# Kernel optimization log

Hardware: AMD Instinct MI355X
Metric: run time of the kernel (lower is better)

Reference implementation:

```python
import jax, jax.numpy as jnp
import numpy as np

B, T, D, F, E = 4, 8192, 1024, 4096, 8


def setup_inputs() -> dict:
    key = jax.random.key(0)
    ks = jax.random.split(key, 5)
    s = 0.02
    return {
        "X": jax.random.normal(ks[0], (B, T, D), dtype=jnp.float32),
        "slots_w": jax.random.normal(ks[1], (E, D), dtype=jnp.float32) * s,
        "w1": jax.random.normal(ks[2], (E, F, D), dtype=jnp.float32) * s,
        "w3": jax.random.normal(ks[3], (E, F, D), dtype=jnp.float32) * s,
        "w2": jax.random.normal(ks[4], (E, D, F), dtype=jnp.float32) * s,
    }


def reference(X, slots_w, w1, w3, w2):
    # logits: [B,T,E]
    logits = jnp.einsum("btd,ed->bte", X, slots_w)
    dispatch_w = jax.nn.softmax(logits, axis=1)  # softmax over tokens
    combine_w = jax.nn.softmax(logits, axis=2)   # softmax over experts
    # slots: one D-vector per expert per batch -> [B,E,D]
    slots = jnp.einsum("bte,btd->bed", dispatch_w, X)
    # SwiGLU FFN batched over experts
    h = jax.nn.silu(jnp.einsum("bed,efd->bef", slots, w1)) * jnp.einsum("bed,efd->bef", slots, w3)
    y = jnp.einsum("bef,edf->bed", h, w2)  # [B,E,D]
    # combine back to tokens: [B,T,D]
    return jnp.einsum("bte,bed->btd", combine_w, y)
```

## Files before the change

kernel.cpp:

```cpp
#include <hip/hip_runtime.h>
#include <math.h>

#define NB 4
#define NT 8192
#define ND 1024
#define NF 4096
#define NE 8

#define DCH 128
#define DTOK 64
#define K7_CHB 256
#define K7_TOK (NT / K7_CHB)

typedef float v4f __attribute__((ext_vector_type(4)));

__device__ __forceinline__ float4 ntload4(const float* p) {
  v4f v = __builtin_nontemporal_load((const v4f*)p);
  return make_float4(v.x, v.y, v.z, v.w);
}
__device__ __forceinline__ void ntstore4(float* p, float4 a) {
  v4f v = {a.x, a.y, a.z, a.w};
  __builtin_nontemporal_store(v, (v4f*)p);
}

__device__ __forceinline__ float dot4(float4 a, float4 b) {
  return a.x * b.x + a.y * b.y + a.z * b.z + a.w * b.w;
}

__device__ __forceinline__ float reduce8(float v0, float v1, float v2, float v3,
                                         float v4, float v5, float v6, float v7,
                                         int lane) {
  const bool b0 = lane & 1;
  float s, u0, u1, u2, u3;
  s = b0 ? v0 : v1; u0 = (b0 ? v1 : v0) + __shfl_xor(s, 1);
  s = b0 ? v2 : v3; u1 = (b0 ? v3 : v2) + __shfl_xor(s, 1);
  s = b0 ? v4 : v5; u2 = (b0 ? v5 : v4) + __shfl_xor(s, 1);
  s = b0 ? v6 : v7; u3 = (b0 ? v7 : v6) + __shfl_xor(s, 1);
  const bool b1 = lane & 2;
  float w0, w1;
  s = b1 ? u0 : u1; w0 = (b1 ? u1 : u0) + __shfl_xor(s, 2);
  s = b1 ? u2 : u3; w1 = (b1 ? u3 : u2) + __shfl_xor(s, 2);
  const bool b2 = lane & 4;
  s = b2 ? w0 : w1; float x = (b2 ? w1 : w0) + __shfl_xor(s, 4);
  x += __shfl_xor(x, 8);
  x += __shfl_xor(x, 16);
  x += __shfl_xor(x, 32);
  return x;
}

__global__ __launch_bounds__(256, 2) void k_dispatch(const float* __restrict__ X,
                                                     const float* __restrict__ sw,
                                                     float* __restrict__ logits,
                                                     float* __restrict__ partial,
                                                     float* __restrict__ Lpart) {
  const int tid = threadIdx.x;
  const int lane = tid & 63, wave = tid >> 6;
  const int b = blockIdx.x >> 7;
  const int chunk = blockIdx.x & 127;
  const int t0 = chunk * DTOK;

  float4 swr[NE];
#pragma unroll
  for (int e = 0; e < NE; ++e)
    swr[e] = *(const float4*)(sw + (size_t)e * ND + tid * 4);

  __shared__ float wred[4][8][8];
  __shared__ float pwt[8][8];
  __shared__ float lsum[8][8];

  const float* xb = X + ((size_t)b * NT + t0) * ND + tid * 4;
  float4 Xc[8], Xn[8];
#pragma unroll
  for (int k = 0; k < 8; ++k) Xc[k] = ntload4(xb + (size_t)k * ND);

  float4 acc[NE];
#pragma unroll
  for (int e = 0; e < NE; ++e) acc[e] = make_float4(0.f, 0.f, 0.f, 0.f);
  float Lacc = 0.f;

  for (int g = 0; g < 8; ++g) {
    if (g < 7) {
#pragma unroll
      for (int k = 0; k < 8; ++k)
        Xn[k] = ntload4(xb + (size_t)((g + 1) * 8 + k) * ND);
    }
#pragma unroll
    for (int k = 0; k < 8; ++k) {
      float p0 = dot4(Xc[k], swr[0]), p1 = dot4(Xc[k], swr[1]);
      float p2 = dot4(Xc[k], swr[2]), p3 = dot4(Xc[k], swr[3]);
      float p4 = dot4(Xc[k], swr[4]), p5 = dot4(Xc[k], swr[5]);
      float p6 = dot4(Xc[k], swr[6]), p7 = dot4(Xc[k], swr[7]);
      float r = reduce8(p0, p1, p2, p3, p4, p5, p6, p7, lane);
      if (lane < 8) wred[wave][k][lane] = r;
    }
    asm volatile("s_waitcnt lgkmcnt(0)" ::: "memory");
    __builtin_amdgcn_s_barrier();
    if (wave == 0) {
      const int t = lane >> 3, e = lane & 7;
      if (lane < 64) {
        float lg = wred[0][t][e] + wred[1][t][e] + wred[2][t][e] + wred[3][t][e];
        logits[((size_t)b * NT + t0 + g * 8 + t) * NE + e] = lg;
        float ex = expf(lg);
        pwt[t][e] = ex;
        Lacc += ex;
      }
    }
    asm volatile("s_waitcnt lgkmcnt(0)" ::: "memory");
    __builtin_amdgcn_s_barrier();
#pragma unroll
    for (int k = 0; k < 8; ++k) {
      float4 pa = *(const float4*)&pwt[k][0];
      float4 pb = *(const float4*)&pwt[k][4];
      float4 x = Xc[k];
      acc[0].x += pa.x * x.x; acc[0].y += pa.x * x.y; acc[0].z += pa.x * x.z; acc[0].w += pa.x * x.w;
      acc[1].x += pa.y * x.x; acc[1].y += pa.y * x.y; acc[1].z += pa.y * x.z; acc[1].w += pa.y * x.w;
      acc[2].x += pa.z * x.x; acc[2].y += pa.z * x.y; acc[2].z += pa.z * x.z; acc[2].w += pa.z * x.w;
      acc[3].x += pa.w * x.x; acc[3].y += pa.w * x.y; acc[3].z += pa.w * x.z; acc[3].w += pa.w * x.w;
      acc[4].x += pb.x * x.x; acc[4].y += pb.x * x.y; acc[4].z += pb.x * x.z; acc[4].w += pb.x * x.w;
      acc[5].x += pb.y * x.x; acc[5].y += pb.y * x.y; acc[5].z += pb.y * x.z; acc[5].w += pb.y * x.w;
      acc[6].x += pb.z * x.x; acc[6].y += pb.z * x.y; acc[6].z += pb.z * x.z; acc[6].w += pb.z * x.w;
      acc[7].x += pb.w * x.x; acc[7].y += pb.w * x.y; acc[7].z += pb.w * x.z; acc[7].w += pb.w * x.w;
    }
    asm volatile("s_waitcnt lgkmcnt(0)" ::: "memory");
    __builtin_amdgcn_s_barrier();
#pragma unroll
    for (int k = 0; k < 8; ++k) Xc[k] = Xn[k];
  }

  float* pout = partial + (size_t)blockIdx.x * (NE * ND) + tid * 4;
#pragma unroll
  for (int e = 0; e < NE; ++e) *(float4*)(pout + e * ND) = acc[e];

  if (wave == 0 && lane < 64) lsum[lane >> 3][lane & 7] = Lacc;
  __syncthreads();
  if (tid < 8) {
    float s = 0.f;
#pragma unroll
    for (int t = 0; t < 8; ++t) s += lsum[t][tid];
    Lpart[(size_t)blockIdx.x * NE + tid] = s;
  }
}

__global__ __launch_bounds__(256, 4) void k_slots_reduce(const float* __restrict__ partial,
                                                         const float* __restrict__ Lpart,
                                                         float* __restrict__ slots) {
  const int col = blockIdx.x * 256 + threadIdx.x;
  const int b = col >> 13;
  const int ed = col & 8191;
  const int e = ed >> 10;
  const float* p = partial + (size_t)b * DCH * (NE * ND) + ed;
  float s = 0.f;
#pragma unroll 8
  for (int c = 0; c < DCH; ++c) s += p[(size_t)c * NE * ND];
  const float* lp = Lpart + (size_t)b * DCH * NE + e;
  float Ls = 0.f;
#pragma unroll 8
  for (int c = 0; c < DCH; ++c) Ls += lp[c * NE];
  slots[col] = s / Ls;
}

__global__ __launch_bounds__(256, 8) void k_ffn1(const float* __restrict__ slots,
                                                 const float* __restrict__ w1,
                                                 const float* __restrict__ w3,
                                                 float* __restrict__ h) {
  __shared__ float4 s_sl[NB][ND / 4];
  const int tid = threadIdx.x;
  const int lane = tid & 63, wave = tid >> 6;
  const int e = blockIdx.x >> 8;
  const int f0 = (blockIdx.x & 255) * 16;
  for (int i = tid; i < NB * ND / 4; i += 256) {
    const int b = i >> 8, j = i & 255;
    s_sl[b][j] = ((const float4*)(slots + ((size_t)b * NE + e) * ND))[j];
  }
  __syncthreads();

  const float* w1e = w1 + (size_t)e * NF * ND;
  const float* w3e = w3 + (size_t)e * NF * ND;
  float4 W1c[4], W3c[4], W1n[4], W3n[4];
  {
    const int f = f0 + wave;
    const float* r1 = w1e + (size_t)f * ND;
    const float* r3 = w3e + (size_t)f * ND;
#pragma unroll
    for (int it = 0; it < 4; ++it) {
      W1c[it] = ntload4(r1 + (it * 64 + lane) * 4);
      W3c[it] = ntload4(r3 + (it * 64 + lane) * 4);
    }
  }
#pragma unroll
  for (int rg = 0; rg < 4; ++rg) {
    const int f = f0 + wave + rg * 4;
    if (rg < 3) {
      const float* r1 = w1e + (size_t)(f + 4) * ND;
      const float* r3 = w3e + (size_t)(f + 4) * ND;
#pragma unroll
      for (int it = 0; it < 4; ++it) {
        W1n[it] = ntload4(r1 + (it * 64 + lane) * 4);
        W3n[it] = ntload4(r3 + (it * 64 + lane) * 4);
      }
    }
    float a1[NB] = {0.f, 0.f, 0.f, 0.f}, a3[NB] = {0.f, 0.f, 0.f, 0.f};
#pragma unroll
    for (int it = 0; it < 4; ++it) {
      float4 x1 = W1c[it], x3 = W3c[it];
#pragma unroll
      for (int b = 0; b < NB; ++b) {
        float4 s = s_sl[b][it * 64 + lane];
        a1[b] += dot4(x1, s);
        a3[b] += dot4(x3, s);
      }
    }
    float x = reduce8(a1[0], a1[1], a1[2], a1[3],
                      a3[0], a3[1], a3[2], a3[3], lane);
    float other = __shfl_xor(x, 4);
    if (lane < 4) {
      const float sil = x / (1.f + expf(-x));
      h[((size_t)e * NB + lane) * NF + f] = sil * other;
    }
#pragma unroll
    for (int it = 0; it < 4; ++it) { W1c[it] = W1n[it]; W3c[it] = W3n[it]; }
  }
}

__global__ __launch_bounds__(256, 4) void k_ffn2(const float* __restrict__ h,
                                                 const float* __restrict__ w2,
                                                 float* __restrict__ y_part) {
  const int tid = threadIdx.x;
  const int lane = tid & 63, wave = tid >> 6;
  const int e = blockIdx.x >> 8;
  const int rem = blockIdx.x & 255;
  const int d0 = (rem >> 2) * 16;
  const int c = rem & 3;
  const int fb = c * 1024;

  const float* he = h + (size_t)e * NB * NF;
  const float* w2e = w2 + (size_t)e * ND * NF;
  const int r0 = d0 + wave * 4;

  float4 Wc[4], Wn[4], Hc[4], Hn[4];
  {
    const int pos = fb + lane * 4;
#pragma unroll
    for (int r = 0; r < 4; ++r) Wc[r] = ntload4(w2e + (size_t)(r0 + r) * NF + pos);
#pragma unroll
    for (int b = 0; b < NB; ++b) Hc[b] = *(const float4*)(he + (size_t)b * NF + pos);
  }
  float acc[4][NB];
#pragma unroll
  for (int r = 0; r < 4; ++r)
#pragma unroll
    for (int b = 0; b < NB; ++b) acc[r][b] = 0.f;

#pragma unroll
  for (int si = 0; si < 4; ++si) {
    if (si < 3) {
      const int pos = fb + (si + 1) * 256 + lane * 4;
#pragma unroll
      for (int r = 0; r < 4; ++r) Wn[r] = ntload4(w2e + (size_t)(r0 + r) * NF + pos);
#pragma unroll
      for (int b = 0; b < NB; ++b) Hn[b] = *(const float4*)(he + (size_t)b * NF + pos);
    }
#pragma unroll
    for (int r = 0; r < 4; ++r)
#pragma unroll
      for (int b = 0; b < NB; ++b) acc[r][b] += dot4(Wc[r], Hc[b]);
#pragma unroll
    for (int r = 0; r < 4; ++r) Wc[r] = Wn[r];
#pragma unroll
    for (int b = 0; b < NB; ++b) Hc[b] = Hn[b];
  }

  float x01 = reduce8(acc[0][0], acc[0][1], acc[0][2], acc[0][3],
                      acc[1][0], acc[1][1], acc[1][2], acc[1][3], lane);
  float x23 = reduce8(acc[2][0], acc[2][1], acc[2][2], acc[2][3],
                      acc[3][0], acc[3][1], acc[3][2], acc[3][3], lane);
  if (lane < 8) {
    const int b = lane & 3, r = lane >> 2;
    y_part[(((size_t)c * NB + b) * NE + e) * ND + r0 + r] = x01;
    y_part[(((size_t)c * NB + b) * NE + e) * ND + r0 + 2 + r] = x23;
  }
}

__global__ __launch_bounds__(256, 4) void k_combine(const float* __restrict__ logits,
                                                    const float* __restrict__ y_part,
                                                    float* __restrict__ out) {
  const int b = blockIdx.x >> 8;
  const int t0 = (blockIdx.x & 255) * K7_TOK;
  __shared__ float4 s_y[NE * ND / 4];
  const float4* yp = (const float4*)y_part;
  for (int i = threadIdx.x; i < NE * ND / 4; i += 256) {
    float4 a = yp[(size_t)(0 * NB + b) * 2048 + i];
    float4 c1 = yp[(size_t)(1 * NB + b) * 2048 + i];
    float4 c2 = yp[(size_t)(2 * NB + b) * 2048 + i];
    float4 c3 = yp[(size_t)(3 * NB + b) * 2048 + i];
    a.x += c1.x + c2.x + c3.x; a.y += c1.y + c2.y + c3.y;
    a.z += c1.z + c2.z + c3.z; a.w += c1.w + c2.w + c3.w;
    s_y[i] = a;
  }
  __shared__ float s_cw[K7_TOK][NE];
  if (threadIdx.x < K7_TOK) {
    const int t = t0 + threadIdx.x;
    const float* lg = logits + ((size_t)b * NT + t) * NE;
    float l[NE];
    float mx = -1e30f;
#pragma unroll
    for (int e = 0; e < NE; ++e) { l[e] = lg[e]; mx = fmaxf(mx, l[e]); }
    float s = 0.f;
#pragma unroll
    for (int e = 0; e < NE; ++e) { l[e] = expf(l[e] - mx); s += l[e]; }
    const float inv = 1.f / s;
#pragma unroll
    for (int e = 0; e < NE; ++e) s_cw[threadIdx.x][e] = l[e] * inv;
  }
  __syncthreads();
  for (int t = 0; t < K7_TOK; ++t) {
    float4 o = make_float4(0.f, 0.f, 0.f, 0.f);
#pragma unroll
    for (int e = 0; e < NE; ++e) {
      const float cw = s_cw[t][e];
      float4 yv = s_y[e * 256 + threadIdx.x];
      o.x += cw * yv.x; o.y += cw * yv.y; o.z += cw * yv.z; o.w += cw * yv.w;
    }
    ntstore4(out + ((size_t)b * NT + t0 + t) * ND + threadIdx.x * 4, o);
  }
}

extern "C" void kernel_launch(void* const* d_in, const int* in_sizes, int n_in,
                              void* d_out, int out_size, void* d_ws, size_t ws_size,
                              hipStream_t stream) {
  const float* X  = (const float*)d_in[0];
  const float* sw = (const float*)d_in[1];
  const float* w1 = (const float*)d_in[2];
  const float* w3 = (const float*)d_in[3];
  const float* w2 = (const float*)d_in[4];
  float* out = (float*)d_out;

  float* ws = (float*)d_ws;
  float* logits  = ws;
  float* partial = logits + (size_t)NB * NT * NE;
  float* Lpart   = partial + (size_t)NB * DCH * NE * ND;
  float* slots   = Lpart + (size_t)NB * DCH * NE;
  float* h       = slots + NB * NE * ND;
  float* y_part  = h + (size_t)NE * NB * NF;

  hipLaunchKernelGGL(k_dispatch, dim3(NB * DCH), dim3(256), 0, stream,
                     X, sw, logits, partial, Lpart);
  hipLaunchKernelGGL(k_slots_reduce, dim3(NB * NE * ND / 256), dim3(256), 0, stream,
                     partial, Lpart, slots);
  hipLaunchKernelGGL(k_ffn1, dim3(NE * (NF / 16)), dim3(256), 0, stream,
                     slots, w1, w3, h);
  hipLaunchKernelGGL(k_ffn2, dim3(NE * (ND / 16) * 4), dim3(256), 0, stream, h, w2, y_part);
  hipLaunchKernelGGL(k_combine, dim3(NB * K7_CHB), dim3(256), 0, stream, logits, y_part, out);
}
```

Baseline: 167.7 us.

## Double-buffer dispatch weights, keep combine y in registers, relax ffn1 launch bounds

In the dispatch kernel, the per-group exp weights go into a two-slot shared buffer, which lets the trailing barrier of each group iteration be removed. The combine kernel now holds the reduced expert outputs in registers per thread instead of staging them in shared memory, and reads the combine weights as vector loads. The occupancy hint on the first FFN kernel drops from 8 to 4 blocks per CU, giving it more registers. These are independent changes across three kernels. Removing the barrier relies on the double buffer preventing a write-after-read race on wred and pwt, and the lower occupancy may reduce latency hiding in ffn1.

```diff
diff --git a/kernel.cpp b/kernel.cpp
--- a/kernel.cpp
+++ b/kernel.cpp
@@ -65,7 +65,7 @@
     swr[e] = *(const float4*)(sw + (size_t)e * ND + tid * 4);
 
   __shared__ float wred[4][8][8];
-  __shared__ float pwt[8][8];
+  __shared__ float pwt[2][8][8];
   __shared__ float lsum[8][8];
 
   const float* xb = X + ((size_t)b * NT + t0) * ND + tid * 4;
@@ -79,6 +79,7 @@
   float Lacc = 0.f;
 
   for (int g = 0; g < 8; ++g) {
+    const int pb = g & 1;
     if (g < 7) {
 #pragma unroll
       for (int k = 0; k < 8; ++k)
@@ -97,32 +98,28 @@
     __builtin_amdgcn_s_barrier();
     if (wave == 0) {
       const int t = lane >> 3, e = lane & 7;
-      if (lane < 64) {
-        float lg = wred[0][t][e] + wred[1][t][e] + wred[2][t][e] + wred[3][t][e];
-        logits[((size_t)b * NT + t0 + g * 8 + t) * NE + e] = lg;
-        float ex = expf(lg);
-        pwt[t][e] = ex;
-        Lacc += ex;
-      }
+      float lg = wred[0][t][e] + wred[1][t][e] + wred[2][t][e] + wred[3][t][e];
+      logits[((size_t)b * NT + t0 + g * 8 + t) * NE + e] = lg;
+      float ex = expf(lg);
+      pwt[pb][t][e] = ex;
+      Lacc += ex;
     }
     asm volatile("s_waitcnt lgkmcnt(0)" ::: "memory");
     __builtin_amdgcn_s_barrier();
 #pragma unroll
     for (int k = 0; k < 8; ++k) {
-      float4 pa = *(const float4*)&pwt[k][0];
-      float4 pb = *(const float4*)&pwt[k][4];
+      float4 pa = *(const float4*)&pwt[pb][k][0];
+      float4 pbv = *(const float4*)&pwt[pb][k][4];
       float4 x = Xc[k];
       acc[0].x += pa.x * x.x; acc[0].y += pa.x * x.y; acc[0].z += pa.x * x.z; acc[0].w += pa.x * x.w;
       acc[1].x += pa.y * x.x; acc[1].y += pa.y * x.y; acc[1].z += pa.y * x.z; acc[1].w += pa.y * x.w;
       acc[2].x += pa.z * x.x; acc[2].y += pa.z * x.y; acc[2].z += pa.z * x.z; acc[2].w += pa.z * x.w;
       acc[3].x += pa.w * x.x; acc[3].y += pa.w * x.y; acc[3].z += pa.w * x.z; acc[3].w += pa.w * x.w;
-      acc[4].x += pb.x * x.x; acc[4].y += pb.x * x.y; acc[4].z += pb.x * x.z; acc[4].w += pb.x * x.w;
-      acc[5].x += pb.y * x.x; acc[5].y += pb.y * x.y; acc[5].z += pb.y * x.z; acc[5].w += pb.y * x.w;
-      acc[6].x += pb.z * x.x; acc[6].y += pb.z * x.y; acc[6].z += pb.z * x.z; acc[6].w += pb.z * x.w;
-      acc[7].x += pb.w * x.x; acc[7].y += pb.w * x.y; acc[7].z += pb.w * x.z; acc[7].w += pb.w * x.w;
-    }
-    asm volatile("s_waitcnt lgkmcnt(0)" ::: "memory");
-    __builtin_amdgcn_s_barrier();
+      acc[4].x += pbv.x * x.x; acc[4].y += pbv.x * x.y; acc[4].z += pbv.x * x.z; acc[4].w += pbv.x * x.w;
+      acc[5].x += pbv.y * x.x; acc[5].y += pbv.y * x.y; acc[5].z += pbv.y * x.z; acc[5].w += pbv.y * x.w;
+      acc[6].x += pbv.z * x.x; acc[6].y += pbv.z * x.y; acc[6].z += pbv.z * x.z; acc[6].w += pbv.z * x.w;
+      acc[7].x += pbv.w * x.x; acc[7].y += pbv.w * x.y; acc[7].z += pbv.w * x.z; acc[7].w += pbv.w * x.w;
+    }
 #pragma unroll
     for (int k = 0; k < 8; ++k) Xc[k] = Xn[k];
   }
@@ -131,7 +128,7 @@
 #pragma unroll
   for (int e = 0; e < NE; ++e) *(float4*)(pout + e * ND) = acc[e];
 
-  if (wave == 0 && lane < 64) lsum[lane >> 3][lane & 7] = Lacc;
+  if (wave == 0) lsum[lane >> 3][lane & 7] = Lacc;
   __syncthreads();
   if (tid < 8) {
     float s = 0.f;
@@ -159,7 +156,7 @@
   slots[col] = s / Ls;
 }
 
-__global__ __launch_bounds__(256, 8) void k_ffn1(const float* __restrict__ slots,
+__global__ __launch_bounds__(256, 4) void k_ffn1(const float* __restrict__ slots,
                                                  const float* __restrict__ w1,
                                                  const float* __restrict__ w3,
                                                  float* __restrict__ h) {
@@ -286,20 +283,24 @@
                                                     float* __restrict__ out) {
   const int b = blockIdx.x >> 8;
   const int t0 = (blockIdx.x & 255) * K7_TOK;
-  __shared__ float4 s_y[NE * ND / 4];
+  const int tid = threadIdx.x;
+
+  float4 yreg[NE];
   const float4* yp = (const float4*)y_part;
-  for (int i = threadIdx.x; i < NE * ND / 4; i += 256) {
-    float4 a = yp[(size_t)(0 * NB + b) * 2048 + i];
-    float4 c1 = yp[(size_t)(1 * NB + b) * 2048 + i];
-    float4 c2 = yp[(size_t)(2 * NB + b) * 2048 + i];
-    float4 c3 = yp[(size_t)(3 * NB + b) * 2048 + i];
+#pragma unroll
+  for (int e = 0; e < NE; ++e) {
+    float4 a = yp[(size_t)((0 * NB + b) * NE + e) * 256 + tid];
+    float4 c1 = yp[(size_t)((1 * NB + b) * NE + e) * 256 + tid];
+    float4 c2 = yp[(size_t)((2 * NB + b) * NE + e) * 256 + tid];
+    float4 c3 = yp[(size_t)((3 * NB + b) * NE + e) * 256 + tid];
     a.x += c1.x + c2.x + c3.x; a.y += c1.y + c2.y + c3.y;
     a.z += c1.z + c2.z + c3.z; a.w += c1.w + c2.w + c3.w;
-    s_y[i] = a;
-  }
+    yreg[e] = a;
+  }
+
   __shared__ float s_cw[K7_TOK][NE];
-  if (threadIdx.x < K7_TOK) {
-    const int t = t0 + threadIdx.x;
+  if (tid < K7_TOK) {
+    const int t = t0 + tid;
     const float* lg = logits + ((size_t)b * NT + t) * NE;
     float l[NE];
     float mx = -1e30f;
@@ -310,18 +311,23 @@
     for (int e = 0; e < NE; ++e) { l[e] = expf(l[e] - mx); s += l[e]; }
     const float inv = 1.f / s;
 #pragma unroll
-    for (int e = 0; e < NE; ++e) s_cw[threadIdx.x][e] = l[e] * inv;
+    for (int e = 0; e < NE; ++e) s_cw[tid][e] = l[e] * inv;
   }
   __syncthreads();
+
   for (int t = 0; t < K7_TOK; ++t) {
+    float4 ca = *(const float4*)&s_cw[t][0];
+    float4 cb = *(const float4*)&s_cw[t][4];
     float4 o = make_float4(0.f, 0.f, 0.f, 0.f);
-#pragma unroll
-    for (int e = 0; e < NE; ++e) {
-      const float cw = s_cw[t][e];
-      float4 yv = s_y[e * 256 + threadIdx.x];
-      o.x += cw * yv.x; o.y += cw * yv.y; o.z += cw * yv.z; o.w += cw * yv.w;
-    }
-    ntstore4(out + ((size_t)b * NT + t0 + t) * ND + threadIdx.x * 4, o);
+    o.x = ca.x * yreg[0].x + ca.y * yreg[1].x + ca.z * yreg[2].x + ca.w * yreg[3].x
+        + cb.x * yreg[4].x + cb.y * yreg[5].x + cb.z * yreg[6].x + cb.w * yreg[7].x;
+    o.y = ca.x * yreg[0].y + ca.y * yreg[1].y + ca.z * yreg[2].y + ca.w * yreg[3].y
+        + cb.x * yreg[4].y + cb.y * yreg[5].y + cb.z * yreg[6].y + cb.w * yreg[7].y;
+    o.z = ca.x * yreg[0].z + ca.y * yreg[1].z + ca.z * yreg[2].z + ca.w * yreg[3].z
+        + cb.x * yreg[4].z + cb.y * yreg[5].z + cb.z * yreg[6].z + cb.w * yreg[7].z;
+    o.w = ca.x * yreg[0].w + ca.y * yreg[1].w + ca.z * yreg[2].w + ca.w * yreg[3].w
+        + cb.x * yreg[4].w + cb.y * yreg[5].w + cb.z * yreg[6].w + cb.w * yreg[7].w;
+    ntstore4(out + ((size_t)b * NT + t0 + t) * ND + tid * 4, o);
   }
 }
 
```

Result: faster. 160.1 us (-4.5%).
